# Kernel optimization log

Hardware: AMD Instinct MI355X
Metric: run time of the kernel (lower is better)

Reference implementation:

```python
import jax, jax.numpy as jnp
import numpy as np

# Model dims (match init_kwargs)
B, L, DH = 4, 1024, 2048
D = 128          # head_dim
HQ, HK, HV = 16, 4, 4
H = 16           # expanded_num_heads = max(HQ, HK, HV)
K = 4            # short conv kernel size
EPS = 1e-5


def causal_depthwise_conv_silu(x, w):
    """ShortConvolution: causal depthwise conv1d + SiLU. x: [B,L,C], w: [C,K]."""
    Lx = x.shape[1]
    xp = jnp.pad(x, ((0, 0), (K - 1, 0), (0, 0)))
    y = sum(xp[:, j:j + Lx] * w[:, j] for j in range(K))
    return jax.nn.silu(y)


def _l2norm(t):
    return t * jax.lax.rsqrt(jnp.sum(t * t, axis=-1, keepdims=True) + 1e-6)


def setup_inputs() -> dict:
    key = jax.random.key(0)
    ks = jax.random.split(key, 14)
    s = 0.02
    # dt_bias init per module: dt ~ logspace(1e-3, 1e-1), inv softplus
    u = jax.random.uniform(ks[7], (H,))
    dt = jnp.exp(u * (np.log(0.1) - np.log(0.001)) + np.log(0.001))
    dt = jnp.clip(dt, 1e-4)
    dt_bias = dt + jnp.log(-jnp.expm1(-dt))
    return {
        "hidden_states": jax.random.normal(ks[0], (B, L, DH), jnp.float32),
        "Wq": jax.random.normal(ks[1], (DH, HQ * D), jnp.float32) * s,
        "Wk": jax.random.normal(ks[2], (DH, HK * D), jnp.float32) * s,
        "Wv": jax.random.normal(ks[3], (DH, HV * D), jnp.float32) * s,
        "Wb": jax.random.normal(ks[4], (DH, H), jnp.float32) * s,
        "Wgk": jax.random.normal(ks[5], (DH, H), jnp.float32) * s,
        "A_log": jnp.log(jax.random.uniform(ks[6], (H,), minval=1e-3, maxval=16.0)),
        "dt_bias": dt_bias,
        "conv_q": jax.random.normal(ks[8], (HQ * D, K), jnp.float32) * 0.1,
        "conv_k": jax.random.normal(ks[9], (HK * D, K), jnp.float32) * 0.1,
        "conv_v": jax.random.normal(ks[10], (HV * D, K), jnp.float32) * 0.1,
        "Wg": jax.random.normal(ks[11], (DH, H * D), jnp.float32) * s,
        "o_norm_w": jnp.ones((D,), jnp.float32),
        "Wo": jax.random.normal(ks[12], (H * D, DH), jnp.float32) * s,
    }


def reference(hidden_states, Wq, Wk, Wv, Wb, Wgk, A_log, dt_bias,
              conv_q, conv_k, conv_v, Wg, o_norm_w, Wo):
    x = hidden_states                                   # [B,L,DH]
    # projections + short causal conv + silu
    q = causal_depthwise_conv_silu(x @ Wq, conv_q).reshape(B, L, HQ, D)
    k = causal_depthwise_conv_silu(x @ Wk, conv_k).reshape(B, L, HK, D)
    v = causal_depthwise_conv_silu(x @ Wv, conv_v).reshape(B, L, HV, D)
    # GQA expansion: '... h d -> ... (h g) d' == repeat each head g times
    k = jnp.repeat(k, H // HK, axis=2)                  # [B,L,H,D]
    v = jnp.repeat(v, H // HV, axis=2)
    # gating scalars
    beta = jax.nn.sigmoid(x @ Wb)                       # [B,L,H]
    g = -jnp.exp(A_log) * jax.nn.softplus(x @ Wgk + dt_bias)  # [B,L,H] (log decay <= 0)
    # qk l2-norm (as in kernel), q scaled by D**-0.5
    q = _l2norm(q) * (D ** -0.5)
    k = _l2norm(k)
    # gated delta-rule recurrence: S_t = exp(g_t) S_{t-1} + beta_t k_t (v_t - k_t^T exp(g_t) S_{t-1})
    qT = q.transpose(1, 0, 2, 3)                        # [L,B,H,D]
    kT = k.transpose(1, 0, 2, 3)
    vT = v.transpose(1, 0, 2, 3)
    gT = g.transpose(1, 0, 2)                           # [L,B,H]
    bT = beta.transpose(1, 0, 2)

    def step(S, inp):
        q_t, k_t, v_t, g_t, b_t = inp
        S = S * jnp.exp(g_t)[..., None, None]           # decay state [B,H,D,D]
        v_res = v_t - jnp.einsum('bhk,bhkv->bhv', k_t, S)
        S = S + b_t[..., None, None] * (k_t[..., None] * v_res[:, :, None, :])
        o_t = jnp.einsum('bhk,bhkv->bhv', q_t, S)
        return S, o_t

    S0 = jnp.zeros((B, H, D, D), jnp.float32)
    _, oT = jax.lax.scan(step, S0, (qT, kT, vT, gT, bT))
    o = oT.transpose(1, 0, 2, 3)                        # [B,L,H,D]
    # FusedRMSNormGated: rmsnorm(o) * w * silu(gate), then output projection
    gate = (x @ Wg).reshape(B, L, H, D)
    o = o * jax.lax.rsqrt(jnp.mean(o * o, axis=-1, keepdims=True) + EPS)
    o = o * o_norm_w * jax.nn.silu(gate)
    return o.reshape(B, L, H * D) @ Wo                  # [B,L,DH]
```

## Files before the change

### kernel.cpp

```cpp
#include <hip/hip_runtime.h>
#include <hip/hip_bf16.h>
#include <math.h>

#define Bb 4
#define Ls 1024
#define DHc 2048
#define Dh 128
#define HQc 16
#define HKc 4
#define Hc 16
#define Mrows 4096
#define CC 64
#define NCH 16

typedef __attribute__((ext_vector_type(8))) short bf16x8;
typedef __attribute__((ext_vector_type(4))) float f32x4;

__device__ inline unsigned short f2b(float f) {
    __hip_bfloat16 h = __float2bfloat16(f);
    return *(unsigned short*)&h;
}
__device__ inline float b2f(unsigned short u) {
    __hip_bfloat16 h = *(__hip_bfloat16*)&u;
    return __bfloat162float(h);
}
__device__ inline bf16x8 scale_frag(bf16x8 a, float s) {
    union { bf16x8 v; unsigned short u[8]; } x;
    x.v = a;
#pragma unroll
    for (int i = 0; i < 8; i++) x.u[i] = f2b(b2f(x.u[i]) * s);
    return x.v;
}

__device__ inline void load_lds16(const void* g, void* l) {
    __builtin_amdgcn_global_load_lds((const __attribute__((address_space(1))) void*)g,
                                     (__attribute__((address_space(3))) void*)l, 16, 0, 0);
}

__device__ inline void bar_lds() {
    asm volatile("s_waitcnt lgkmcnt(0)" ::: "memory");
    __builtin_amdgcn_s_barrier();
    asm volatile("" ::: "memory");
}

__global__ void f32_to_bf16(const float* __restrict__ in, __hip_bfloat16* __restrict__ out, int n)
{
    int i = (blockIdx.x * 256 + threadIdx.x) * 4;
    if (i >= n) return;
    float4 v = *(const float4*)(in + i);
    __hip_bfloat16 h[4];
    h[0] = __float2bfloat16(v.x); h[1] = __float2bfloat16(v.y);
    h[2] = __float2bfloat16(v.z); h[3] = __float2bfloat16(v.w);
    *(uint2*)(out + i) = *(uint2*)h;
}

__launch_bounds__(256)
__global__ void transpose_to_bf16(const float* __restrict__ W, __hip_bfloat16* __restrict__ BT,
                                  int Krows, int Ncols)
{
    __shared__ float tile[64][65];
    const int n0 = blockIdx.x * 64, k0 = blockIdx.y * 64;
    const int tx = threadIdx.x & 63, ty = threadIdx.x >> 6;
#pragma unroll
    for (int r = ty; r < 64; r += 4)
        tile[r][tx] = W[(size_t)(k0 + r) * Ncols + n0 + tx];
    __syncthreads();
#pragma unroll
    for (int r = ty; r < 64; r += 4)
        BT[(size_t)(n0 + r) * Krows + k0 + tx] = __float2bfloat16(tile[tx][r]);
}

__launch_bounds__(256)
__global__ void transpose_all_bf16(const float* __restrict__ Wq, const float* __restrict__ Wk,
                                   const float* __restrict__ Wv, const float* __restrict__ Wg,
                                   __hip_bfloat16* __restrict__ BTall)
{
    const int lb = blockIdx.x;
    const float* W; __hip_bfloat16* BT; int Ncols, bx, by;
    if (lb < 1024)      { W = Wq; BT = BTall;                          Ncols = 2048; int r = lb;        bx = r & 31; by = r >> 5; }
    else if (lb < 1280) { W = Wk; BT = BTall + (size_t)2048 * 2048;    Ncols = 512;  int r = lb - 1024; bx = r & 7;  by = r >> 3; }
    else if (lb < 1536) { W = Wv; BT = BTall + (size_t)2560 * 2048;    Ncols = 512;  int r = lb - 1280; bx = r & 7;  by = r >> 3; }
    else                { W = Wg; BT = BTall + (size_t)3072 * 2048;    Ncols = 2048; int r = lb - 1536; bx = r & 31; by = r >> 5; }

    __shared__ float tile[64][65];
    const int n0 = bx * 64, k0 = by * 64;
    const int tx = threadIdx.x & 63, ty = threadIdx.x >> 6;
#pragma unroll
    for (int r = ty; r < 64; r += 4)
        tile[r][tx] = W[(size_t)(k0 + r) * Ncols + n0 + tx];
    __syncthreads();
#pragma unroll
    for (int r = ty; r < 64; r += 4)
        BT[(size_t)(n0 + r) * 2048 + k0 + tx] = __float2bfloat16(tile[tx][r]);
}

__launch_bounds__(256)
__global__ void gemm_bt_n64_f32(const __hip_bfloat16* __restrict__ A, const __hip_bfloat16* __restrict__ BT,
                                float* __restrict__ C, int N, int K)
{
    __shared__ __align__(16) unsigned short As[128 * 32];
    __shared__ __align__(16) unsigned short Bs[64 * 32];
    const int tid = threadIdx.x;
    const int lane = tid & 63;
    const int wave = tid >> 6;
    const int wm = (wave >> 1) * 64, wn = (wave & 1) * 32;
    const int row0 = blockIdx.y * 128, col0 = blockIdx.x * 64;

    const int rA0 = wave * 16 + (lane >> 2);
    const int rA1 = 64 + wave * 16 + (lane >> 2);
    const int rB  = wave * 16 + (lane >> 2);
    const int kk = ((lane & 3) ^ ((lane >> 3) & 3)) * 8;
    const __hip_bfloat16* Ap0 = A + (size_t)(row0 + rA0) * K + kk;
    const __hip_bfloat16* Ap1 = A + (size_t)(row0 + rA1) * K + kk;
    const __hip_bfloat16* Bp0 = BT + (size_t)(col0 + rB) * K + kk;
    unsigned short* sa0 = &As[(wave * 16) * 32];
    unsigned short* sa1 = &As[(64 + wave * 16) * 32];
    unsigned short* sb0 = &Bs[(wave * 16) * 32];

    f32x4 acc[4][2];
#pragma unroll
    for (int i = 0; i < 4; i++)
#pragma unroll
        for (int j = 0; j < 2; j++) acc[i][j] = (f32x4){0.f, 0.f, 0.f, 0.f};

    const int fr = lane & 15;
    const int fs = (((lane >> 4) ^ ((fr >> 1) & 3))) * 8;

    for (int k0 = 0; k0 < K; k0 += 32) {
        __syncthreads();
        load_lds16(Ap0, sa0);
        load_lds16(Ap1, sa1);
        load_lds16(Bp0, sb0);
        Ap0 += 32; Ap1 += 32; Bp0 += 32;
        __syncthreads();

        bf16x8 af[4], bfr[2];
#pragma unroll
        for (int i = 0; i < 4; i++)
            af[i] = *(const bf16x8*)&As[(wm + i * 16 + fr) * 32 + fs];
#pragma unroll
        for (int j = 0; j < 2; j++)
            bfr[j] = *(const bf16x8*)&Bs[(wn + j * 16 + fr) * 32 + fs];
#pragma unroll
        for (int i = 0; i < 4; i++)
#pragma unroll
            for (int j = 0; j < 2; j++)
                acc[i][j] = __builtin_amdgcn_mfma_f32_16x16x32_bf16(af[i], bfr[j], acc[i][j], 0, 0, 0);
    }

    const int cr = (lane >> 4) * 4;
    const int cc = lane & 15;
#pragma unroll
    for (int i = 0; i < 4; i++)
#pragma unroll
        for (int j = 0; j < 2; j++) {
            size_t base = (size_t)(row0 + wm + i * 16 + cr) * N + (col0 + wn + j * 16 + cc);
#pragma unroll
            for (int p = 0; p < 4; p++)
                C[base + (size_t)p * N] = acc[i][j][p];
        }
}

__launch_bounds__(256)
__global__ void gemm_proj_fused(const __hip_bfloat16* __restrict__ A, const __hip_bfloat16* __restrict__ BT,
                                __hip_bfloat16* __restrict__ preQ, __hip_bfloat16* __restrict__ preK,
                                __hip_bfloat16* __restrict__ preV, __hip_bfloat16* __restrict__ gate)
{
    const int K = 2048;
    __shared__ __align__(16) unsigned short As[128 * 32];
    __shared__ __align__(16) unsigned short Bs[128 * 32];
    const int tid = threadIdx.x;
    const int lane = tid & 63;
    const int wave = tid >> 6;
    const int wm = (wave >> 1) * 64, wn = (wave & 1) * 64;
    const int row0 = blockIdx.y * 128;
    const int cb = blockIdx.x;
    const int col0 = cb * 128;

    __hip_bfloat16* Cb; int Nloc, c0loc;
    if (cb < 16)      { Cb = preQ; Nloc = 2048; c0loc = cb * 128; }
    else if (cb < 20) { Cb = preK; Nloc = 512;  c0loc = (cb - 16) * 128; }
    else if (cb < 24) { Cb = preV; Nloc = 512;  c0loc = (cb - 20) * 128; }
    else              { Cb = gate; Nloc = 2048; c0loc = (cb - 24) * 128; }

    const int r0 = (wave * 2 + 0) * 16 + (lane >> 2);
    const int r1 = (wave * 2 + 1) * 16 + (lane >> 2);
    const int kk = ((lane & 3) ^ ((lane >> 3) & 3)) * 8;
    const __hip_bfloat16* Ap0 = A + (size_t)(row0 + r0) * K + kk;
    const __hip_bfloat16* Ap1 = A + (size_t)(row0 + r1) * K + kk;
    const __hip_bfloat16* Bp0 = BT + (size_t)(col0 + r0) * K + kk;
    const __hip_bfloat16* Bp1 = BT + (size_t)(col0 + r1) * K + kk;
    unsigned short* sa0 = &As[(wave * 2 + 0) * 16 * 32];
    unsigned short* sa1 = &As[(wave * 2 + 1) * 16 * 32];
    unsigned short* sb0 = &Bs[(wave * 2 + 0) * 16 * 32];
    unsigned short* sb1 = &Bs[(wave * 2 + 1) * 16 * 32];

    f32x4 acc[4][4];
#pragma unroll
    for (int i = 0; i < 4; i++)
#pragma unroll
        for (int j = 0; j < 4; j++) acc[i][j] = (f32x4){0.f, 0.f, 0.f, 0.f};

    const int fr = lane & 15;
    const int fs = (((lane >> 4) ^ ((fr >> 1) & 3))) * 8;

    for (int k0 = 0; k0 < K; k0 += 32) {
        __syncthreads();
        load_lds16(Ap0, sa0);
        load_lds16(Ap1, sa1);
        load_lds16(Bp0, sb0);
        load_lds16(Bp1, sb1);
        Ap0 += 32; Ap1 += 32; Bp0 += 32; Bp1 += 32;
        __syncthreads();

        bf16x8 af[4], bfr[4];
#pragma unroll
        for (int i = 0; i < 4; i++)
            af[i] = *(const bf16x8*)&As[(wm + i * 16 + fr) * 32 + fs];
#pragma unroll
        for (int j = 0; j < 4; j++)
            bfr[j] = *(const bf16x8*)&Bs[(wn + j * 16 + fr) * 32 + fs];
#pragma unroll
        for (int i = 0; i < 4; i++)
#pragma unroll
            for (int j = 0; j < 4; j++)
                acc[i][j] = __builtin_amdgcn_mfma_f32_16x16x32_bf16(af[i], bfr[j], acc[i][j], 0, 0, 0);
    }

    const int cr = (lane >> 4) * 4;
    const int cc = lane & 15;
#pragma unroll
    for (int i = 0; i < 4; i++)
#pragma unroll
        for (int j = 0; j < 4; j++) {
            size_t base = (size_t)(row0 + wm + i * 16 + cr) * Nloc + (c0loc + wn + j * 16 + cc);
#pragma unroll
            for (int p = 0; p < 4; p++)
                Cb[base + (size_t)p * Nloc] = __float2bfloat16(acc[i][j][p]);
        }
}

__global__ void conv_silu_norm(const __hip_bfloat16* __restrict__ pre, const float* __restrict__ w,
                               __hip_bfloat16* __restrict__ out, int NH, int do_norm, float scale)
{
    __shared__ float red[2];
    const int idx = blockIdx.x;
    const int head = idx % NH;
    const int l = (idx / NH) % Ls;
    const int b = idx / (NH * Ls);
    const int C = NH * Dh;
    const int c = head * Dh + threadIdx.x;
    const __hip_bfloat16* base = pre + ((size_t)b * Ls + l) * C + c;
    const float4 wv = *(const float4*)(w + (size_t)c * 4);

    float v0 = (l >= 3) ? __bfloat162float(base[-3 * C]) : 0.f;
    float v1 = (l >= 2) ? __bfloat162float(base[-2 * C]) : 0.f;
    float v2 = (l >= 1) ? __bfloat162float(base[-1 * C]) : 0.f;
    float v3 = __bfloat162float(base[0]);
    float y = v0 * wv.x + v1 * wv.y + v2 * wv.z + v3 * wv.w;
    y = y / (1.f + expf(-y));

    if (do_norm) {
        float ss = y * y;
#pragma unroll
        for (int off = 32; off > 0; off >>= 1) ss += __shfl_xor(ss, off);
        if ((threadIdx.x & 63) == 0) red[threadIdx.x >> 6] = ss;
        __syncthreads();
        float tot = red[0] + red[1];
        y = y * rsqrtf(tot + 1e-6f) * scale;
    }
    out[((size_t)b * Ls + l) * C + c] = __float2bfloat16(y);
}

__global__ void pack_wt32(const float* __restrict__ Wb, const float* __restrict__ Wgk,
                          __hip_bfloat16* __restrict__ WT)
{
    const int t = blockIdx.x * 64 + (threadIdx.x & 63);
    const int h0 = (threadIdx.x >> 6) * 4;
#pragma unroll
    for (int i = 0; i < 4; i++) {
        const int h = h0 + i;
        WT[(size_t)h * 2048 + t]        = __float2bfloat16(Wb[(size_t)t * 16 + h]);
        WT[(size_t)(16 + h) * 2048 + t] = __float2bfloat16(Wgk[(size_t)t * 16 + h]);
    }
}

__launch_bounds__(256)
__global__ void proj_bg(const __hip_bfloat16* __restrict__ xbf, const __hip_bfloat16* __restrict__ WT32,
                        const float* __restrict__ A_log, const float* __restrict__ dt_bias,
                        float* __restrict__ beta, float* __restrict__ g)
{
    const int tid = threadIdx.x;
    const int lane = tid & 63;
    const int wave = tid >> 6;
    const int q = lane >> 4;
    const int cL = lane & 15;
    const int row0 = blockIdx.x * 64 + wave * 16;

    const unsigned short* xu = (const unsigned short*)xbf;
    const unsigned short* wu = (const unsigned short*)WT32;

    f32x4 accB = (f32x4){0.f, 0.f, 0.f, 0.f};
    f32x4 accG = (f32x4){0.f, 0.f, 0.f, 0.f};
    const size_t arow = (size_t)(row0 + cL) * 2048;
    const size_t brow = (size_t)cL * 2048;
    const size_t grow = (size_t)(16 + cL) * 2048;

#pragma unroll 4
    for (int k = 0; k < 2048; k += 32) {
        bf16x8 af  = *(const bf16x8*)&xu[arow + k + q * 8];
        bf16x8 wbf = *(const bf16x8*)&wu[brow + k + q * 8];
        bf16x8 wgf = *(const bf16x8*)&wu[grow + k + q * 8];
        accB = __builtin_amdgcn_mfma_f32_16x16x32_bf16(af, wbf, accB, 0, 0, 0);
        accG = __builtin_amdgcn_mfma_f32_16x16x32_bf16(af, wgf, accG, 0, 0, 0);
    }

    const float al = __expf(A_log[cL]);
    const float db = dt_bias[cL];
#pragma unroll
    for (int p = 0; p < 4; p++) {
        const int r = row0 + 4 * q + p;
        beta[(size_t)r * 16 + cL] = 1.f / (1.f + __expf(-accB[p]));
        float z = accG[p] + db;
        float sp = (z > 20.f) ? z : log1pf(__expf(z));
        g[(size_t)r * 16 + cL] = -al * sp;
    }
}

__global__ void bcum_kernel(const float* __restrict__ g, float* __restrict__ bcum)
{
    const int c = blockIdx.x & 15;
    const int bh = blockIdx.x >> 4;
    const int b = bh >> 4;
    const int h = bh & 15;
    const int t = threadIdx.x;
    float v = g[((size_t)(b * Ls + c * CC + t)) * 16 + h];
#pragma unroll
    for (int d = 1; d < 64; d <<= 1) {
        float n = __shfl_up(v, d, 64);
        if (t >= d) v += n;
    }
    bcum[(size_t)blockIdx.x * 64 + t] = v;
}

__launch_bounds__(256)
__global__ void gdn_phase1(const __hip_bfloat16* __restrict__ kc, const __hip_bfloat16* __restrict__ vc,
                           const float* __restrict__ bb, const float* __restrict__ bcum,
                           __hip_bfloat16* __restrict__ U, __hip_bfloat16* __restrict__ Z)
{
    const int task = blockIdx.x;
    const int c = task & 15;
    const int bh = task >> 4;
    const int b = bh >> 4;
    const int h = bh & 15;
    const int hk = h >> 2;
    const int tid = threadIdx.x;
    const int lane = tid & 63;
    const int wave = tid >> 6;
    const int q = lane >> 4;
    const int cL = lane & 15;

    __shared__ float Ab[64][68];
    __shared__ float sbeta[64], sbc[64];

    if (tid < 64) {
        sbeta[tid] = bb[((size_t)(b * Ls + c * CC + tid)) * 16 + h];
        sbc[tid] = bcum[((size_t)bh * 16 + c) * 64 + tid];
    }
    __syncthreads();

    const unsigned short* ku = (const unsigned short*)kc;
    const unsigned short* vu = (const unsigned short*)vc;

    f32x4 pacc[4];
#pragma unroll
    for (int j = 0; j < 4; j++) pacc[j] = (f32x4){0.f, 0.f, 0.f, 0.f};
    {
        const int t = 16 * wave + cL;
        const size_t krow = (((size_t)(b * Ls + c * CC + t)) * 4 + hk) * 128;
#pragma unroll
        for (int ks = 0; ks < 4; ks++) {
            bf16x8 af = *(const bf16x8*)&ku[krow + ks * 32 + q * 8];
#pragma unroll
            for (int j = 0; j < 4; j++) {
                const int s = 16 * j + cL;
                bf16x8 bf = *(const bf16x8*)&ku[(((size_t)(b * Ls + c * CC + s)) * 4 + hk) * 128 + ks * 32 + q * 8];
                pacc[j] = __builtin_amdgcn_mfma_f32_16x16x32_bf16(af, bf, pacc[j], 0, 0, 0);
            }
        }
    }
#pragma unroll
    for (int j = 0; j < 4; j++)
#pragma unroll
        for (int p = 0; p < 4; p++) {
            const int t = 16 * wave + 4 * q + p;
            const int s = 16 * j + cL;
            float val = 0.f;
            if (s < t) val = sbeta[t] * __expf(sbc[t] - sbc[s]) * pacc[j][p];
            Ab[t][s] = val;
        }
    __syncthreads();

    float u[64];
    const int j = tid;
    if (j < 128) {
#pragma unroll
        for (int t = 0; t < 64; t++)
            u[t] = sbeta[t] * b2f(vu[(((size_t)(b * Ls + c * CC + t)) * 4 + hk) * 128 + j]);
    } else {
        const int k = j - 128;
#pragma unroll
        for (int t = 0; t < 64; t++)
            u[t] = sbeta[t] * __expf(sbc[t]) * b2f(ku[(((size_t)(b * Ls + c * CC + t)) * 4 + hk) * 128 + k]);
    }
#pragma unroll
    for (int t = 1; t < 64; t++) {
        const float4* ar = (const float4*)Ab[t];
        const int nf = (t + 3) >> 2;
        float a0 = 0.f, a1 = 0.f, a2 = 0.f, a3 = 0.f;
#pragma unroll
        for (int i = 0; i < nf; i++) {
            float4 av = ar[i];
            a0 = fmaf(av.x, u[4 * i + 0], a0);
            a1 = fmaf(av.y, u[4 * i + 1], a1);
            a2 = fmaf(av.z, u[4 * i + 2], a2);
            a3 = fmaf(av.w, u[4 * i + 3], a3);
        }
        u[t] -= (a0 + a1) + (a2 + a3);
    }
    const size_t slab = ((size_t)bh * 16 + c) * 8192;
    if (j < 128) {
        unsigned short* Up = (unsigned short*)U + slab + (size_t)j * 64;
#pragma unroll
        for (int t8 = 0; t8 < 8; t8++) {
            union { bf16x8 v; unsigned short us[8]; } pk;
#pragma unroll
            for (int e = 0; e < 8; e++) pk.us[e] = f2b(u[8 * t8 + e]);
            *(bf16x8*)&Up[t8 * 8] = pk.v;
        }
    } else {
#pragma unroll
        for (int t = 0; t < 64; t++) Z[slab + t * 128 + (j - 128)] = __float2bfloat16(u[t]);
    }
}

__launch_bounds__(256, 1)
__global__ void gdn_phase2(const __hip_bfloat16* __restrict__ qc, const __hip_bfloat16* __restrict__ kc,
                           __hip_bfloat16* Uw ,
                           const __hip_bfloat16* __restrict__ Zbuf,
                           const float* __restrict__ bcum, float* __restrict__ Obuf)
{
    const int blk = blockIdx.x;
    const int quarter = blk & 3;
    const int bh = blk >> 2;
    const int b = bh >> 4;
    const int h = bh & 15;
    const int hk = h >> 2;
    const int vbase = quarter * 32;
    const int tid = threadIdx.x;
    const int lane = tid & 63;
    const int wave = tid >> 6;
    const int q = lane >> 4;
    const int cL = lane & 15;

    __shared__ __align__(16) unsigned short Tb[32 * 136];
    __shared__ __align__(16) unsigned short Kt[128 * 72];
    __shared__ __align__(16) unsigned short Wt[32 * 72];
    __shared__ __align__(16) unsigned short Us[32 * 72];

    const unsigned short* qu = (const unsigned short*)qc;
    const unsigned short* ku = (const unsigned short*)kc;
    unsigned short* Uu = (unsigned short*)Uw;
    const unsigned short* Zu = (const unsigned short*)Zbuf;

    const int tloc = tid & 63;
    const int kg = tid >> 6;
    const int trow = 16 * wave + cL;
    const int wv = (wave & 1) * 16;
    const int wk = (wave >> 1) * 4;

    f32x4 Tacc[4];
#pragma unroll
    for (int j = 0; j < 4; j++) Tacc[j] = (f32x4){0.f, 0.f, 0.f, 0.f};

    bf16x8 Kreg[4], Zreg[4], Qreg[4];
    uint4 Ureg;
    float p_bctl, p_bc63;
    float4 p_bct4;

    auto prefetch = [&](int c) {
        const size_t base_t = (size_t)b * Ls + (size_t)c * CC;
        const size_t slab = ((size_t)bh * 16 + c) * 8192;
        const size_t krow = ((base_t + tloc) * 4 + hk) * 128 + 32 * kg;
#pragma unroll
        for (int m = 0; m < 4; m++) Kreg[m] = *(const bf16x8*)&ku[krow + m * 8];
        Ureg = *(const uint4*)&Uu[slab + (size_t)(vbase + (tid >> 3)) * 64 + (tid & 7) * 8];
        const size_t zrow = slab + (size_t)trow * 128;
        const size_t qrow = ((base_t + trow) * 16 + h) * 128;
#pragma unroll
        for (int ks = 0; ks < 4; ks++) {
            Zreg[ks] = *(const bf16x8*)&Zu[zrow + ks * 32 + q * 8];
            Qreg[ks] = *(const bf16x8*)&qu[qrow + ks * 32 + q * 8];
        }
        const float* bc = bcum + ((size_t)bh * 16 + c) * 64;
        p_bctl = bc[tloc];
        p_bc63 = bc[63];
        p_bct4 = *(const float4*)&bc[16 * wave + 4 * q];
    };

    prefetch(0);

    for (int c = 0; c < NCH; ++c) {
        bf16x8 kr[4], zr[4], qr[4];
        uint4 ur;
#pragma unroll
        for (int m = 0; m < 4; m++) { kr[m] = Kreg[m]; zr[m] = Zreg[m]; qr[m] = Qreg[m]; }
        ur = Ureg;
        const float bctl = p_bctl, bc63 = p_bc63;
        const float4 bct4 = p_bct4;
        const size_t slab = ((size_t)bh * 16 + c) * 8192;

        if (c + 1 < NCH) prefetch(c + 1);

        const float ek = __expf(bc63 - bctl);
        const float eC = __expf(bc63);

        bar_lds();

#pragma unroll
        for (int m = 0; m < 4; m++) {
            union { bf16x8 v; unsigned short us[8]; } kv;
            kv.v = scale_frag(kr[m], ek);
#pragma unroll
            for (int e = 0; e < 8; e++) Kt[(32 * kg + 8 * m + e) * 72 + tloc] = kv.us[e];
        }
        *(uint4*)&Us[(tid >> 3) * 72 + (tid & 7) * 8] = ur;
#pragma unroll
        for (int j = 0; j < 4; j++)
#pragma unroll
            for (int p = 0; p < 4; p++)
                Tb[(wv + 4 * q + p) * 136 + (wave >> 1) * 64 + 16 * j + cL] = f2b(Tacc[j][p]);

        bar_lds();

        f32x4 Wacc[2], Oacc[2];
#pragma unroll
        for (int j = 0; j < 2; j++) { Wacc[j] = (f32x4){0.f,0.f,0.f,0.f}; Oacc[j] = (f32x4){0.f,0.f,0.f,0.f}; }
#pragma unroll
        for (int ks = 0; ks < 4; ks++) {
#pragma unroll
            for (int j = 0; j < 2; j++) {
                bf16x8 bt = *(const bf16x8*)&Tb[(16 * j + cL) * 136 + 32 * ks + 8 * q];
                Wacc[j] = __builtin_amdgcn_mfma_f32_16x16x32_bf16(zr[ks], bt, Wacc[j], 0, 0, 0);
                Oacc[j] = __builtin_amdgcn_mfma_f32_16x16x32_bf16(qr[ks], bt, Oacc[j], 0, 0, 0);
            }
        }
        float e4[4] = {__expf(bct4.x), __expf(bct4.y), __expf(bct4.z), __expf(bct4.w)};
#pragma unroll
        for (int j = 0; j < 2; j++)
#pragma unroll
            for (int p = 0; p < 4; p++) {
                const int t = 16 * wave + 4 * q + p;
                const int v = 16 * j + cL;
                const float w = b2f(Us[v * 72 + t]) - Wacc[j][p];
                Wt[v * 72 + t] = f2b(w);
                Obuf[((size_t)b * Ls + c * CC + t) * 2048 + h * 128 + vbase + v] = Oacc[j][p] * e4[p];
            }

        bar_lds();

        {
            const int vloc = tid >> 3, part = tid & 7;
            const size_t dst = slab + (size_t)(vbase + vloc) * 64 + part * 8;
            *(uint4*)&Uu[dst] = *(const uint4*)&Wt[vloc * 72 + part * 8];
        }
#pragma unroll
        for (int j = 0; j < 4; j++)
#pragma unroll
            for (int p = 0; p < 4; p++) Tacc[j][p] *= eC;
#pragma unroll
        for (int ks = 0; ks < 2; ks++) {
            bf16x8 aw = *(const bf16x8*)&Wt[(wv + cL) * 72 + 32 * ks + 8 * q];
#pragma unroll
            for (int j = 0; j < 4; j++) {
                bf16x8 bk = *(const bf16x8*)&Kt[((wk + j) * 16 + cL) * 72 + 32 * ks + 8 * q];
                Tacc[j] = __builtin_amdgcn_mfma_f32_16x16x32_bf16(aw, bk, Tacc[j], 0, 0, 0);
            }
        }
    }
}

__launch_bounds__(256)
__global__ void gdn_phase3(const __hip_bfloat16* __restrict__ qc, const __hip_bfloat16* __restrict__ kc,
                           const __hip_bfloat16* __restrict__ WT, const float* __restrict__ bcum,
                           const float* __restrict__ Obuf, const __hip_bfloat16* __restrict__ gate,
                           const float* __restrict__ onw, __hip_bfloat16* __restrict__ nrm)
{
    const int task = blockIdx.x;
    const int c = task & 15;
    const int bh = task >> 4;
    const int b = bh >> 4;
    const int h = bh & 15;
    const int hk = h >> 2;
    const int tid = threadIdx.x;
    const int lane = tid & 63;
    const int wave = tid >> 6;
    const int q = lane >> 4;
    const int cL = lane & 15;

    __shared__ __align__(16) unsigned short Mb[64 * 72];
    __shared__ float sbc[64];

    if (tid < 64) sbc[tid] = bcum[((size_t)bh * 16 + c) * 64 + tid];
    __syncthreads();

    const unsigned short* qu = (const unsigned short*)qc;
    const unsigned short* ku = (const unsigned short*)kc;
    const unsigned short* wu = (const unsigned short*)WT;
    const unsigned short* gu = (const unsigned short*)gate;
    unsigned short* nu = (unsigned short*)nrm;

    f32x4 pacc[4];
#pragma unroll
    for (int j = 0; j < 4; j++) pacc[j] = (f32x4){0.f, 0.f, 0.f, 0.f};
    {
        const int t = 16 * wave + cL;
        const size_t qrow = (((size_t)(b * Ls + c * CC + t)) * 16 + h) * 128;
#pragma unroll
        for (int ks = 0; ks < 4; ks++) {
            bf16x8 aq = *(const bf16x8*)&qu[qrow + ks * 32 + q * 8];
#pragma unroll
            for (int j = 0; j < 4; j++) {
                const int s = 16 * j + cL;
                bf16x8 bk = *(const bf16x8*)&ku[(((size_t)(b * Ls + c * CC + s)) * 4 + hk) * 128 + ks * 32 + q * 8];
                pacc[j] = __builtin_amdgcn_mfma_f32_16x16x32_bf16(aq, bk, pacc[j], 0, 0, 0);
            }
        }
    }
#pragma unroll
    for (int j = 0; j < 4; j++)
#pragma unroll
        for (int p = 0; p < 4; p++) {
            const int t = 16 * wave + 4 * q + p;
            const int s = 16 * j + cL;
            const float val = (s <= t) ? __expf(sbc[t] - sbc[s]) * pacc[j][p] : 0.f;
            Mb[t * 72 + s] = f2b(val);
        }
    __syncthreads();

    f32x4 oacc[8];
#pragma unroll
    for (int j = 0; j < 8; j++) oacc[j] = (f32x4){0.f, 0.f, 0.f, 0.f};
    const size_t slab = ((size_t)bh * 16 + c) * 8192;
#pragma unroll
    for (int ks = 0; ks < 2; ks++) {
        bf16x8 am = *(const bf16x8*)&Mb[(16 * wave + cL) * 72 + ks * 32 + q * 8];
#pragma unroll
        for (int j = 0; j < 8; j++) {
            const int v = 16 * j + cL;
            bf16x8 bw = *(const bf16x8*)&wu[slab + (size_t)v * 64 + ks * 32 + q * 8];
            oacc[j] = __builtin_amdgcn_mfma_f32_16x16x32_bf16(am, bw, oacc[j], 0, 0, 0);
        }
    }

#pragma unroll
    for (int p = 0; p < 4; p++) {
        const int t = 16 * wave + 4 * q + p;
        const size_t l = (size_t)(b * Ls + c * CC + t);
        const size_t orow = l * 2048 + (size_t)h * 128;
        const size_t xrow = (l * 16 + h) * 128;
        float ov[8];
        float ss = 0.f;
#pragma unroll
        for (int j = 0; j < 8; j++) {
            const int v = 16 * j + cL;
            ov[j] = Obuf[orow + v] + oacc[j][p];
            ss += ov[j] * ov[j];
        }
#pragma unroll
        for (int m = 1; m < 16; m <<= 1) ss += __shfl_xor(ss, m);
        const float r = rsqrtf(ss * (1.f / 128.f) + 1e-5f);
#pragma unroll
        for (int j = 0; j < 8; j++) {
            const int v = 16 * j + cL;
            const float gv = b2f(gu[xrow + v]);
            nu[xrow + v] = f2b(ov[j] * r * onw[v] * (gv / (1.f + __expf(-gv))));
        }
    }
}

extern "C" void kernel_launch(void* const* d_in, const int* in_sizes, int n_in,
                              void* d_out, int out_size, void* d_ws, size_t ws_size,
                              hipStream_t stream)
{
    const float* x     = (const float*)d_in[0];
    const float* Wq    = (const float*)d_in[1];
    const float* Wk    = (const float*)d_in[2];
    const float* Wv    = (const float*)d_in[3];
    const float* Wb    = (const float*)d_in[4];
    const float* Wgk   = (const float*)d_in[5];
    const float* A_log = (const float*)d_in[6];
    const float* dtb   = (const float*)d_in[7];
    const float* cq    = (const float*)d_in[8];
    const float* ck    = (const float*)d_in[9];
    const float* cv    = (const float*)d_in[10];
    const float* Wg    = (const float*)d_in[11];
    const float* onw   = (const float*)d_in[12];
    const float* Wo    = (const float*)d_in[13];

    char* wsb = (char*)d_ws;
    __hip_bfloat16* xbf  = (__hip_bfloat16*)(wsb + 0);
    __hip_bfloat16* qcb  = (__hip_bfloat16*)(wsb + 16777216);
    __hip_bfloat16* kcb  = (__hip_bfloat16*)(wsb + 33554432);
    __hip_bfloat16* vcb  = (__hip_bfloat16*)(wsb + 37748736);
    __hip_bfloat16* Uw   = (__hip_bfloat16*)(wsb + 41943040);
    __hip_bfloat16* Zb   = (__hip_bfloat16*)(wsb + 58720256);
    float*          bcum = (float*)(wsb + 75497472);

    __hip_bfloat16* Zdelta = xbf;
    __hip_bfloat16* nrm    = xbf;

    __hip_bfloat16* BTall = qcb;

    char* dob = (char*)d_out;
    __hip_bfloat16* preQ = (__hip_bfloat16*)dob;
    __hip_bfloat16* preK = (__hip_bfloat16*)(dob + 16777216);
    __hip_bfloat16* preV = (__hip_bfloat16*)(dob + 20971520);
    float* bb = (float*)(dob + 25165824);
    float* gb = (float*)(dob + 25427968);
    __hip_bfloat16* WT32 = (__hip_bfloat16*)(dob + 25690112);
    float* Obuf = (float*)d_out;

    const float qscale = 0.08838834764831845f;
    const int nx = Mrows * DHc;

    f32_to_bf16<<<nx / 4 / 256, 256, 0, stream>>>(x, xbf, nx);
    pack_wt32<<<32, 256, 0, stream>>>(Wb, Wgk, WT32);
    proj_bg<<<64, 256, 0, stream>>>(xbf, WT32, A_log, dtb, bb, gb);
    bcum_kernel<<<64 * NCH, 64, 0, stream>>>(gb, bcum);

    transpose_all_bf16<<<2560, 256, 0, stream>>>(Wq, Wk, Wv, Wg, BTall);

    gemm_proj_fused<<<dim3(40, 32), 256, 0, stream>>>(xbf, BTall, preQ, preK, preV, Zb);

    conv_silu_norm<<<Mrows * HQc, 128, 0, stream>>>(preQ, cq, qcb, HQc, 1, qscale);
    conv_silu_norm<<<Mrows * HKc, 128, 0, stream>>>(preK, ck, kcb, HKc, 1, 1.0f);
    conv_silu_norm<<<Mrows * HKc, 128, 0, stream>>>(preV, cv, vcb, HKc, 0, 1.0f);

    gdn_phase1<<<64 * NCH, 256, 0, stream>>>(kcb, vcb, bb, bcum, Uw, Zdelta);
    gdn_phase2<<<256, 256, 0, stream>>>(qcb, kcb, Uw, Zdelta, bcum, Obuf);
    gdn_phase3<<<64 * NCH, 256, 0, stream>>>(qcb, kcb, Uw, bcum, Obuf, Zb, onw, nrm);

    transpose_to_bf16<<<dim3(32, 32), 256, 0, stream>>>(Wo, (__hip_bfloat16*)Uw, 2048, 2048);
    gemm_bt_n64_f32<<<dim3(32, 32), 256, 0, stream>>>(nrm, (__hip_bfloat16*)Uw, (float*)d_out, 2048, 2048);
}
```

Before: 507.6 us.

## Double GEMM K-tile to 64 and tile conv-silu-norm over 32 timesteps

The fused projection GEMM now stages a K-slice of 64 per iteration instead of 32, with a new XOR swizzle. This halves the number of barrier pairs and loads more per sync, at the cost of doubling LDS use. The conv+silu+norm kernel now has each block walk 32 consecutive timesteps for one head, carrying the three previous inputs in registers instead of re-reading them. This cuts redundant global loads and the block launch count, but reduces parallelism and adds a barrier per timestep.

```diff
diff --git a/kernel.cpp b/kernel.cpp
--- a/kernel.cpp
+++ b/kernel.cpp
@@ -167,8 +167,8 @@
                                 __hip_bfloat16* __restrict__ preV, __hip_bfloat16* __restrict__ gate)
 {
     const int K = 2048;
-    __shared__ __align__(16) unsigned short As[128 * 32];
-    __shared__ __align__(16) unsigned short Bs[128 * 32];
+    __shared__ __align__(16) unsigned short As[128 * 64];
+    __shared__ __align__(16) unsigned short Bs[128 * 64];
     const int tid = threadIdx.x;
     const int lane = tid & 63;
     const int wave = tid >> 6;
@@ -183,17 +183,12 @@
     else if (cb < 24) { Cb = preV; Nloc = 512;  c0loc = (cb - 20) * 128; }
     else              { Cb = gate; Nloc = 2048; c0loc = (cb - 24) * 128; }
 
-    const int r0 = (wave * 2 + 0) * 16 + (lane >> 2);
-    const int r1 = (wave * 2 + 1) * 16 + (lane >> 2);
-    const int kk = ((lane & 3) ^ ((lane >> 3) & 3)) * 8;
-    const __hip_bfloat16* Ap0 = A + (size_t)(row0 + r0) * K + kk;
-    const __hip_bfloat16* Ap1 = A + (size_t)(row0 + r1) * K + kk;
-    const __hip_bfloat16* Bp0 = BT + (size_t)(col0 + r0) * K + kk;
-    const __hip_bfloat16* Bp1 = BT + (size_t)(col0 + r1) * K + kk;
-    unsigned short* sa0 = &As[(wave * 2 + 0) * 16 * 32];
-    unsigned short* sa1 = &As[(wave * 2 + 1) * 16 * 32];
-    unsigned short* sb0 = &Bs[(wave * 2 + 0) * 16 * 32];
-    unsigned short* sb1 = &Bs[(wave * 2 + 1) * 16 * 32];
+    const int rr = lane >> 3;
+    const int kk = ((lane & 7) ^ rr) * 8;
+    const __hip_bfloat16* Ap = A + (size_t)(row0 + wave * 32 + rr) * K + kk;
+    const __hip_bfloat16* Bp = BT + (size_t)(col0 + wave * 32 + rr) * K + kk;
+    unsigned short* saw = &As[wave * 32 * 64];
+    unsigned short* sbw = &Bs[wave * 32 * 64];
 
     f32x4 acc[4][4];
 #pragma unroll
@@ -202,29 +197,35 @@
         for (int j = 0; j < 4; j++) acc[i][j] = (f32x4){0.f, 0.f, 0.f, 0.f};
 
     const int fr = lane & 15;
-    const int fs = (((lane >> 4) ^ ((fr >> 1) & 3))) * 8;
-
-    for (int k0 = 0; k0 < K; k0 += 32) {
+    const int q = lane >> 4;
+    const int rho = fr & 7;
+
+    for (int k0 = 0; k0 < K; k0 += 64) {
         __syncthreads();
-        load_lds16(Ap0, sa0);
-        load_lds16(Ap1, sa1);
-        load_lds16(Bp0, sb0);
-        load_lds16(Bp1, sb1);
-        Ap0 += 32; Ap1 += 32; Bp0 += 32; Bp1 += 32;
+#pragma unroll
+        for (int m = 0; m < 4; m++) {
+            load_lds16(Ap + (size_t)m * 8 * K, saw + m * 8 * 64);
+            load_lds16(Bp + (size_t)m * 8 * K, sbw + m * 8 * 64);
+        }
+        Ap += 64; Bp += 64;
         __syncthreads();
 
-        bf16x8 af[4], bfr[4];
-#pragma unroll
-        for (int i = 0; i < 4; i++)
-            af[i] = *(const bf16x8*)&As[(wm + i * 16 + fr) * 32 + fs];
-#pragma unroll
-        for (int j = 0; j < 4; j++)
-            bfr[j] = *(const bf16x8*)&Bs[(wn + j * 16 + fr) * 32 + fs];
-#pragma unroll
-        for (int i = 0; i < 4; i++)
+#pragma unroll
+        for (int ks = 0; ks < 2; ks++) {
+            const int ps = ((ks * 4 + q) ^ rho) * 8;
+            bf16x8 af[4], bfr[4];
+#pragma unroll
+            for (int i = 0; i < 4; i++)
+                af[i] = *(const bf16x8*)&As[(wm + i * 16 + fr) * 64 + ps];
 #pragma unroll
             for (int j = 0; j < 4; j++)
-                acc[i][j] = __builtin_amdgcn_mfma_f32_16x16x32_bf16(af[i], bfr[j], acc[i][j], 0, 0, 0);
+                bfr[j] = *(const bf16x8*)&Bs[(wn + j * 16 + fr) * 64 + ps];
+#pragma unroll
+            for (int i = 0; i < 4; i++)
+#pragma unroll
+                for (int j = 0; j < 4; j++)
+                    acc[i][j] = __builtin_amdgcn_mfma_f32_16x16x32_bf16(af[i], bfr[j], acc[i][j], 0, 0, 0);
+        }
     }
 
     const int cr = (lane >> 4) * 4;
@@ -240,36 +241,37 @@
         }
 }
 
-__global__ void conv_silu_norm(const __hip_bfloat16* __restrict__ pre, const float* __restrict__ w,
-                               __hip_bfloat16* __restrict__ out, int NH, int do_norm, float scale)
-{
-    __shared__ float red[2];
-    const int idx = blockIdx.x;
-    const int head = idx % NH;
-    const int l = (idx / NH) % Ls;
-    const int b = idx / (NH * Ls);
+__global__ void conv_silu_norm_v2(const __hip_bfloat16* __restrict__ pre, const float* __restrict__ w,
+                                  __hip_bfloat16* __restrict__ out, int NH, int do_norm, float scale)
+{
+    __shared__ float red[2][2];
+    const int head = blockIdx.x;
+    const int r0 = blockIdx.y * 32;
     const int C = NH * Dh;
     const int c = head * Dh + threadIdx.x;
-    const __hip_bfloat16* base = pre + ((size_t)b * Ls + l) * C + c;
     const float4 wv = *(const float4*)(w + (size_t)c * 4);
-
-    float v0 = (l >= 3) ? __bfloat162float(base[-3 * C]) : 0.f;
-    float v1 = (l >= 2) ? __bfloat162float(base[-2 * C]) : 0.f;
-    float v2 = (l >= 1) ? __bfloat162float(base[-1 * C]) : 0.f;
-    float v3 = __bfloat162float(base[0]);
-    float y = v0 * wv.x + v1 * wv.y + v2 * wv.z + v3 * wv.w;
-    y = y / (1.f + expf(-y));
-
-    if (do_norm) {
-        float ss = y * y;
-#pragma unroll
-        for (int off = 32; off > 0; off >>= 1) ss += __shfl_xor(ss, off);
-        if ((threadIdx.x & 63) == 0) red[threadIdx.x >> 6] = ss;
-        __syncthreads();
-        float tot = red[0] + red[1];
-        y = y * rsqrtf(tot + 1e-6f) * scale;
-    }
-    out[((size_t)b * Ls + l) * C + c] = __float2bfloat16(y);
+    const __hip_bfloat16* base = pre + (size_t)r0 * C + c;
+    const bool seqstart = (r0 & (Ls - 1)) == 0;
+
+    float v0 = seqstart ? 0.f : __bfloat162float(base[-3 * (ptrdiff_t)C]);
+    float v1 = seqstart ? 0.f : __bfloat162float(base[-2 * (ptrdiff_t)C]);
+    float v2 = seqstart ? 0.f : __bfloat162float(base[-1 * (ptrdiff_t)C]);
+
+    for (int lt = 0; lt < 32; ++lt) {
+        float v3 = __bfloat162float(base[(size_t)lt * C]);
+        float y = v0 * wv.x + v1 * wv.y + v2 * wv.z + v3 * wv.w;
+        y = y / (1.f + __expf(-y));
+        if (do_norm) {
+            float ss = y * y;
+#pragma unroll
+            for (int off = 32; off > 0; off >>= 1) ss += __shfl_xor(ss, off);
+            if ((threadIdx.x & 63) == 0) red[lt & 1][threadIdx.x >> 6] = ss;
+            __syncthreads();
+            y = y * rsqrtf(red[lt & 1][0] + red[lt & 1][1] + 1e-6f) * scale;
+        }
+        out[(size_t)(r0 + lt) * C + c] = __float2bfloat16(y);
+        v0 = v1; v1 = v2; v2 = v3;
+    }
 }
 
 __global__ void pack_wt32(const float* __restrict__ Wb, const float* __restrict__ Wgk,
@@ -743,9 +745,9 @@
 
     gemm_proj_fused<<<dim3(40, 32), 256, 0, stream>>>(xbf, BTall, preQ, preK, preV, Zb);
 
-    conv_silu_norm<<<Mrows * HQc, 128, 0, stream>>>(preQ, cq, qcb, HQc, 1, qscale);
-    conv_silu_norm<<<Mrows * HKc, 128, 0, stream>>>(preK, ck, kcb, HKc, 1, 1.0f);
-    conv_silu_norm<<<Mrows * HKc, 128, 0, stream>>>(preV, cv, vcb, HKc, 0, 1.0f);
+    conv_silu_norm_v2<<<dim3(HQc, Mrows / 32), 128, 0, stream>>>(preQ, cq, qcb, HQc, 1, qscale);
+    conv_silu_norm_v2<<<dim3(HKc, Mrows / 32), 128, 0, stream>>>(preK, ck, kcb, HKc, 1, 1.0f);
+    conv_silu_norm_v2<<<dim3(HKc, Mrows / 32), 128, 0, stream>>>(preV, cv, vcb, HKc, 0, 1.0f);
 
     gdn_phase1<<<64 * NCH, 256, 0, stream>>>(kcb, vcb, bb, bcum, Uw, Zdelta);
     gdn_phase2<<<256, 256, 0, stream>>>(qcb, kcb, Uw, Zdelta, bcum, Obuf);
```

After: 517.5 us. Within noise of the previous version (+1.9%).
